# Kernel tuning notes

Hardware: AMD Instinct MI355X
Metric: run time of the kernel (lower is better)

## Reference

```python
import jax, jax.numpy as jnp
import numpy as np

B, NX, W, DX, DY, D, H, P = 8, 512, 16, 1536, 1024, 768, 12, 8


def setup_inputs() -> dict:
    key = jax.random.key(0)
    ks = jax.random.split(key, 12)
    r = lambda k, s: jax.random.normal(k, s, dtype=jnp.float32) * 0.02
    return {
        "x": jax.random.normal(ks[0], (B, NX, DX), jnp.float32),
        "y": jax.random.normal(ks[1], (B, NX * W, DY), jnp.float32),
        "Wx": r(ks[2], (DX, D)), "bx": jnp.zeros((D,), jnp.float32),
        "Wy": r(ks[3], (DY, D)), "by": jnp.zeros((D,), jnp.float32),
        "prompt": r(ks[4], (1, P, D)),
        "Wq": r(ks[5], (D, D)), "bq": jnp.zeros((D,), jnp.float32),
        "Wk": r(ks[6], (D, D)), "bk": jnp.zeros((D,), jnp.float32),
        "Wv": r(ks[7], (D, D)), "bv": jnp.zeros((D,), jnp.float32),
        "Wo": r(ks[8], (D, D)), "bo": jnp.zeros((D,), jnp.float32),
        "ln_g": jnp.ones((D,), jnp.float32), "ln_b": jnp.zeros((D,), jnp.float32),
    }


def _l2n(f, eps=1e-6):
    return f / (jnp.linalg.norm(f, axis=-1, keepdims=True) + eps)


def reference(x, y, Wx, bx, Wy, by, prompt, Wq, bq, Wk, bk, Wv, bv, Wo, bo, ln_g, ln_b):
    dh = D // H
    scale = 1.0 / jnp.sqrt(jnp.float32(dh))
    xp = _l2n(x @ Wx + bx)            # [B,NX,D]
    yp = _l2n(y @ Wy + by)            # [B,NX*W,D]
    # In the original, only normalized_output[:,0:1] is kept per window, and
    # per-query attention is independent, so only query index 0 contributes.
    q = ((xp[:, 0] @ Wq) + bq).reshape(B, H, dh) * scale   # [B,H,dh]
    yw = yp.reshape(B, NX, W, D)                            # 16-token windows
    k = ((yw @ Wk) + bk).reshape(B, NX, W, H, dh)
    v = ((yw @ Wv) + bv).reshape(B, NX, W, H, dh)
    s = jnp.einsum('bhd,bnwhd->bhnw', q, k)                # [B,H,NX,W]
    a = jax.nn.softmax(s, axis=-1)
    ctx = jnp.einsum('bhnw,bnwhd->bnhd', a, v).reshape(B, NX, D)
    o = ctx @ Wo + bo                                      # attn out_proj
    mu = jnp.mean(o, axis=-1, keepdims=True)
    var = jnp.var(o, axis=-1, keepdims=True)
    normed = (o - mu) / jnp.sqrt(var + 1e-6) * ln_g + ln_b  # [B,NX,D]
    blocks = jnp.concatenate(
        [normed[:, :, None, :],
         jnp.broadcast_to(prompt[:, None], (B, NX, P, D))], axis=2)  # [B,NX,1+P,D]
    return blocks.reshape(B, NX * (1 + P), D)
```

## Files before the change

kernel.cpp:

```cpp
#include <hip/hip_runtime.h>
#include <stdint.h>

#define BQ 8
#define NXQ 512
#define WQ 16
#define DXQ 1536
#define DYQ 1024
#define DQ 768
#define HQ 12
#define PQ 8
#define MY 65536
#define BN_ROWS 4096

typedef __attribute__((ext_vector_type(8))) short short8;
typedef __attribute__((ext_vector_type(4))) float f32x4;
typedef unsigned short ushort_t;
typedef unsigned int uint_t;

__device__ __forceinline__ ushort_t f2bf(float f) {
  uint_t u = __float_as_uint(f);
  u += 0x7FFFu + ((u >> 16) & 1u);
  return (ushort_t)(u >> 16);
}
__device__ __forceinline__ float bf2f(ushort_t h) {
  return __uint_as_float(((uint_t)h) << 16);
}
__device__ __forceinline__ void gload_lds16(const void* g, void* l) {
  __builtin_amdgcn_global_load_lds(
      (__attribute__((address_space(1))) unsigned int*)(g),
      (__attribute__((address_space(3))) unsigned int*)(l), 16, 0, 0);
}

__global__ void k_conv(const float* __restrict__ y, const float* __restrict__ Wy,
                       const float* __restrict__ Wv, const float* __restrict__ Wo,
                       ushort_t* __restrict__ ybf, ushort_t* __restrict__ WyT,
                       ushort_t* __restrict__ WvT, ushort_t* __restrict__ WoT,
                       float* __restrict__ rowsq, float* __restrict__ oS12,
                       float* __restrict__ xw) {
  const int gstride = gridDim.x * blockDim.x;
  const int g0 = blockIdx.x * blockDim.x + threadIdx.x;
  const int NY8 = MY * DYQ / 8;
  for (int i = g0; i < NY8; i += gstride) {
    const float4* s = (const float4*)(y + (size_t)i * 8);
    float4 f0 = s[0], f1 = s[1];
    short8 hv;
    hv[0] = (short)f2bf(f0.x); hv[1] = (short)f2bf(f0.y);
    hv[2] = (short)f2bf(f0.z); hv[3] = (short)f2bf(f0.w);
    hv[4] = (short)f2bf(f1.x); hv[5] = (short)f2bf(f1.y);
    hv[6] = (short)f2bf(f1.z); hv[7] = (short)f2bf(f1.w);
    *(short8*)(ybf + (size_t)i * 8) = hv;
  }
  for (int i = g0; i < MY; i += gstride) rowsq[i] = 0.f;
  for (int i = g0; i < 2 * BN_ROWS; i += gstride) oS12[i] = 0.f;
  for (int i = g0; i < BQ * DQ; i += gstride) xw[i] = 0.f;
  const int N1 = DQ * DYQ;
  const int N2 = DQ * DQ;
  const int total = N1 + 2 * N2;
  for (int i = g0; i < total; i += gstride) {
    if (i < N1) {
      int n = i / DYQ, k = i - n * DYQ;
      WyT[i] = f2bf(Wy[k * DQ + n]);
    } else if (i < N1 + N2) {
      int j = i - N1;
      int n = j / DQ, k = j - n * DQ;
      WvT[j] = f2bf(Wv[k * DQ + n]);
    } else {
      int j = i - N1 - N2;
      int n = j / DQ, k = j - n * DQ;
      WoT[j] = f2bf(Wo[k * DQ + n]);
    }
  }
}

__global__ __launch_bounds__(128) void k_q1(const float* __restrict__ x,
                                            const float* __restrict__ Wx,
                                            const float* __restrict__ bx,
                                            float* __restrict__ xw) {
  const int b = blockIdx.x, c = blockIdx.y * 128 + threadIdx.x;
  const int kc = blockIdx.z;
  const float* xr = x + (size_t)b * NXQ * DXQ + kc * 192;
  const float* wp = Wx + (size_t)kc * 192 * DQ + c;
  float acc = (kc == 0) ? bx[c] : 0.f;
  for (int k = 0; k < 192; ++k) acc += xr[k] * wp[(size_t)k * DQ];
  atomicAdd(&xw[b * DQ + c], acc);
}

__global__ __launch_bounds__(128) void k_q2(const float* __restrict__ xw,
                                            const float* __restrict__ Wq,
                                            const float* __restrict__ bq,
                                            float* __restrict__ qv) {
  const int b = blockIdx.x, c = blockIdx.y * 128 + threadIdx.x;
  const float* xr = xw + b * DQ;
  float acc = 0.f, ss = 0.f;
  for (int k = 0; k < DQ; ++k) {
    float v = xr[k];
    acc += v * Wq[(size_t)k * DQ + c];
    ss += v * v;
  }
  const float inv = 1.0f / (sqrtf(ss) + 1e-6f);
  qv[b * DQ + c] = (acc * inv + bq[c]) * 0.125f;
}

__global__ void k_q3(const float* __restrict__ Wk, const float* __restrict__ bk,
                     const float* __restrict__ qv, float* __restrict__ qk,
                     float* __restrict__ cQ) {
  const int bh = blockIdx.x;
  const int b = bh / HQ, h = bh - b * HQ;
  const int tid = threadIdx.x;
  const float* q = qv + b * DQ + h * 64;
#pragma unroll
  for (int j = 0; j < 3; ++j) {
    int dd = tid + j * 256;
    float acc = 0.f;
    for (int j2 = 0; j2 < 64; ++j2) acc += Wk[(size_t)dd * DQ + h * 64 + j2] * q[j2];
    qk[(size_t)bh * DQ + dd] = acc;
  }
  if (tid == 0) {
    float acc = 0.f;
    for (int j2 = 0; j2 < 64; ++j2) acc += q[j2] * bk[h * 64 + j2];
    cQ[bh] = acc;
  }
}

__global__ __launch_bounds__(512, 1) void k_gemm_yp(const ushort_t* __restrict__ ybf,
                                                    const ushort_t* __restrict__ WyT,
                                                    const float* __restrict__ by,
                                                    ushort_t* __restrict__ z,
                                                    float* __restrict__ rowsqg) {
  __shared__ __align__(16) char smem[131072 + 1024];
  float* rowsq_l = (float*)(smem + 131072);
  const int tid = threadIdx.x, lane = tid & 63, wv = tid >> 6;
  const int wvM = wv >> 2, wvN = wv & 3;
  const int g = blockIdx.x;
  const int m = (g / 24) * 8 + (g & 7);
  const int n = (g >> 3) % 3;
  const int mBase = m * 256, nBase = n * 256;
  if (tid < 256) rowsq_l[tid] = 0.f;

  const int sr = lane >> 2;
  const int sc = (lane & 3) ^ (sr & 3);
  const ushort_t* aQ[2]; const ushort_t* bQ[2];
  int qDst[2];
#pragma unroll
  for (int j = 0; j < 2; ++j) {
    int r = wv * 32 + j * 16 + sr;
    aQ[j] = ybf + (size_t)(mBase + r) * DYQ + sc * 8;
    bQ[j] = WyT + (size_t)(nBase + r) * DYQ + sc * 8;
    qDst[j] = (wv * 32 + j * 16) * 64;
  }
  const int q = lane >> 4;
  int aFr[8], bFr[4];
#pragma unroll
  for (int mf = 0; mf < 8; ++mf) {
    int r = wvM * 128 + mf * 16 + (lane & 15);
    aFr[mf] = r * 64 + ((q ^ (r & 3)) << 4);
  }
#pragma unroll
  for (int nf = 0; nf < 4; ++nf) {
    int r = wvN * 64 + nf * 16 + (lane & 15);
    bFr[nf] = 32768 + r * 64 + ((q ^ (r & 3)) << 4);
  }

#define YP_STAGE(bufb, tt, ks)                                                 \
  {                                                                            \
    char* db = smem + (bufb) * 65536 + (ks) * 16384;                           \
    _Pragma("unroll") for (int j = 0; j < 2; ++j)                              \
        gload_lds16(aQ[j] + (tt) * 64 + (ks) * 32, db + qDst[j]);              \
    _Pragma("unroll") for (int j = 0; j < 2; ++j)                              \
        gload_lds16(bQ[j] + (tt) * 64 + (ks) * 32, db + 32768 + qDst[j]);      \
  }

  f32x4 acc[8][4] = {};
  YP_STAGE(0, 0, 0);
  YP_STAGE(0, 0, 1);
  for (int t = 0; t < 16; ++t) {
    const int c = t & 1;
    const char* cb = smem + c * 65536;
#pragma unroll
    for (int ks = 0; ks < 2; ++ks) {
      if (t == 15 && ks == 1) {
        asm volatile("s_waitcnt vmcnt(0)" ::: "memory");
      } else {
        asm volatile("s_waitcnt vmcnt(4)" ::: "memory");
      }
      __builtin_amdgcn_s_barrier();
      __builtin_amdgcn_sched_barrier(0);
      short8 af[8], bf[4];
#pragma unroll
      for (int mf = 0; mf < 8; ++mf)
        af[mf] = *(const short8*)(cb + ks * 16384 + aFr[mf]);
#pragma unroll
      for (int nf = 0; nf < 4; ++nf)
        bf[nf] = *(const short8*)(cb + ks * 16384 + bFr[nf]);
      if (t < 15) YP_STAGE(c ^ 1, t + 1, ks);
      asm volatile("s_waitcnt lgkmcnt(0)" ::: "memory");
      __builtin_amdgcn_sched_barrier(0);
      __builtin_amdgcn_s_setprio(1);
#pragma unroll
      for (int nf = 0; nf < 4; ++nf)
#pragma unroll
        for (int mf = 0; mf < 8; ++mf)
          acc[mf][nf] = __builtin_amdgcn_mfma_f32_16x16x32_bf16(af[mf], bf[nf],
                                                                acc[mf][nf], 0, 0, 0);
      __builtin_amdgcn_s_setprio(0);
      __builtin_amdgcn_sched_barrier(0);
    }
  }
  __syncthreads();

  float byv[4];
#pragma unroll
  for (int nf = 0; nf < 4; ++nf) byv[nf] = by[nBase + wvN * 64 + nf * 16 + (lane & 15)];
#pragma unroll
  for (int mf = 0; mf < 8; ++mf) {
#pragma unroll
    for (int rr = 0; rr < 4; ++rr) {
      int row_l = wvM * 128 + mf * 16 + (lane >> 4) * 4 + rr;
      float ss = 0.f;
#pragma unroll
      for (int nf = 0; nf < 4; ++nf) {
        float zv = acc[mf][nf][rr] + byv[nf];
        ss += zv * zv;
        int col_l = wvN * 64 + nf * 16 + (lane & 15);
        *(ushort_t*)(smem + row_l * 512 + col_l * 2) = f2bf(zv);
      }
#pragma unroll
      for (int o = 1; o < 16; o <<= 1) ss += __shfl_xor(ss, o, 64);
      if ((lane & 15) == 0) atomicAdd(&rowsq_l[row_l], ss);
    }
  }
  __syncthreads();
  if (tid < 256) atomicAdd(&rowsqg[mBase + tid], rowsq_l[tid]);
#pragma unroll
  for (int it = 0; it < 16; ++it) {
    int row = it * 16 + (tid >> 5);
    int ch = tid & 31;
    uint4 v = *(const uint4*)(smem + row * 512 + ch * 16);
    *(uint4*)(z + (size_t)(mBase + row) * DQ + nBase + ch * 8) = v;
  }
}

__global__ __launch_bounds__(256) void k_attn(const ushort_t* __restrict__ z,
                                              const float* __restrict__ rowsqg,
                                              const float* __restrict__ qk,
                                              const float* __restrict__ cQ,
                                              ushort_t* __restrict__ p) {
  __shared__ __align__(16) char smem[16 * 1552 + 192 * 4 * 2 + 64];
  float* s_l = (float*)(smem + 16 * 1552);
  float* a_l = s_l + 192;
  float* inv_l = a_l + 192;
  const int bn = blockIdx.x, b = bn >> 9;
  const int tid = threadIdx.x;
  if (tid < 16) inv_l[tid] = 1.0f / (sqrtf(rowsqg[bn * 16 + tid]) + 1e-6f);
  for (int j = tid; j < 16 * 96; j += 256) {
    int w = j / 96, ch = j - w * 96;
    *(short8*)(smem + w * 1552 + ch * 16) =
        *(const short8*)(z + ((size_t)bn * 16 + w) * DQ + ch * 8);
  }
  __syncthreads();
  if (tid < 192) {
    int h = tid >> 4, w = tid & 15;
    const float4* qkp = (const float4*)(qk + (size_t)(b * HQ + h) * DQ);
    float acc = 0.f;
    const char* yrow = smem + w * 1552;
    for (int dc = 0; dc < 192; ++dc) {
      float4 q4 = qkp[dc];
      uint2 hh = *(const uint2*)(yrow + dc * 8);
      acc += q4.x * bf2f((ushort_t)(hh.x & 0xffff));
      acc += q4.y * bf2f((ushort_t)(hh.x >> 16));
      acc += q4.z * bf2f((ushort_t)(hh.y & 0xffff));
      acc += q4.w * bf2f((ushort_t)(hh.y >> 16));
    }
    s_l[tid] = acc * inv_l[w] + cQ[b * HQ + h];
  }
  __syncthreads();
  if (tid < 12) {
    float mx = -1e30f;
#pragma unroll
    for (int w = 0; w < 16; ++w) mx = fmaxf(mx, s_l[tid * 16 + w]);
    float sm = 0.f, ev[16];
#pragma unroll
    for (int w = 0; w < 16; ++w) {
      ev[w] = __expf(s_l[tid * 16 + w] - mx);
      sm += ev[w];
    }
    float rden = 1.0f / sm;
#pragma unroll
    for (int w = 0; w < 16; ++w) a_l[tid * 16 + w] = ev[w] * rden * inv_l[w];
  }
  __syncthreads();
  float zr[16][3];
#pragma unroll
  for (int w = 0; w < 16; ++w)
#pragma unroll
    for (int i = 0; i < 3; ++i)
      zr[w][i] = bf2f(*(const ushort_t*)(smem + w * 1552 + (tid + i * 256) * 2));
  for (int h = 0; h < HQ; ++h) {
    float acc0 = 0.f, acc1 = 0.f, acc2 = 0.f;
#pragma unroll
    for (int w = 0; w < 16; ++w) {
      float aw = a_l[h * 16 + w];
      acc0 += aw * zr[w][0];
      acc1 += aw * zr[w][1];
      acc2 += aw * zr[w][2];
    }
    size_t base = ((size_t)bn * HQ + h) * DQ + tid;
    p[base] = f2bf(acc0);
    p[base + 256] = f2bf(acc1);
    p[base + 512] = f2bf(acc2);
  }
}

#define PV_TSZ 24576
__global__ __launch_bounds__(256) void k_gemm_pv(const ushort_t* __restrict__ p,
                                                 const ushort_t* __restrict__ WvT,
                                                 const float* __restrict__ bv,
                                                 ushort_t* __restrict__ ctx) {
  __shared__ __align__(16) char smem[3 * PV_TSZ];
  const int tid = threadIdx.x, lane = tid & 63, wv = tid >> 6;
  const int wvM = wv >> 1, wvN = wv & 1;
  const int mBase = blockIdx.x * 128, h = blockIdx.y;
  const int l8 = lane >> 3;
  const int c8 = (lane & 7) ^ (l8 & 7);
  const ushort_t* aSrc[4]; const ushort_t* bSrc[2];
  int aDst[4], bDst[2];
#pragma unroll
  for (int j = 0; j < 4; ++j) {
    int r = wv * 32 + j * 8 + l8;
    aSrc[j] = p + ((size_t)(mBase + r) * HQ + h) * DQ + c8 * 8;
    aDst[j] = (wv * 32 + j * 8) * 128;
  }
#pragma unroll
  for (int j = 0; j < 2; ++j) {
    int r = wv * 16 + j * 8 + l8;
    bSrc[j] = WvT + (size_t)(h * 64 + r) * DQ + c8 * 8;
    bDst[j] = 16384 + (wv * 16 + j * 8) * 128;
  }
  const int q = lane >> 4;
  int aRowB[4], aSw[4], bRowB[2], bSw[2];
#pragma unroll
  for (int mf = 0; mf < 4; ++mf) {
    int r = wvM * 64 + mf * 16 + (lane & 15);
    aRowB[mf] = r * 128; aSw[mf] = r & 7;
  }
#pragma unroll
  for (int nf = 0; nf < 2; ++nf) {
    int r = wvN * 32 + nf * 16 + (lane & 15);
    bRowB[nf] = 16384 + r * 128; bSw[nf] = r & 7;
  }
#define PV_STAGE(dbuf, t)                                                      \
  {                                                                            \
    char* db = smem + (dbuf) * PV_TSZ;                                         \
    _Pragma("unroll") for (int j = 0; j < 4; ++j)                              \
        gload_lds16(aSrc[j] + (t) * 64, db + aDst[j]);                         \
    _Pragma("unroll") for (int j = 0; j < 2; ++j)                              \
        gload_lds16(bSrc[j] + (t) * 64, db + bDst[j]);                         \
  }
  f32x4 acc[4][2] = {};
  PV_STAGE(0, 0);
  PV_STAGE(1, 1);
  int bR = 0, bS = 2;
  for (int t = 0; t < 12; ++t) {
    if (t < 11) {
      asm volatile("s_waitcnt vmcnt(6)" ::: "memory");
    } else {
      asm volatile("s_waitcnt vmcnt(0)" ::: "memory");
    }
    __builtin_amdgcn_s_barrier();
    __builtin_amdgcn_sched_barrier(0);
    if (t + 2 < 12) PV_STAGE(bS, t + 2);
    const char* cur = smem + bR * PV_TSZ;
#pragma unroll
    for (int ks = 0; ks < 2; ++ks) {
      short8 af[4], bf[2];
#pragma unroll
      for (int mf = 0; mf < 4; ++mf)
        af[mf] = *(const short8*)(cur + aRowB[mf] + (((ks * 4 + q) ^ aSw[mf]) << 4));
#pragma unroll
      for (int nf = 0; nf < 2; ++nf)
        bf[nf] = *(const short8*)(cur + bRowB[nf] + (((ks * 4 + q) ^ bSw[nf]) << 4));
#pragma unroll
      for (int nf = 0; nf < 2; ++nf)
#pragma unroll
        for (int mf = 0; mf < 4; ++mf)
          acc[mf][nf] = __builtin_amdgcn_mfma_f32_16x16x32_bf16(af[mf], bf[nf],
                                                                acc[mf][nf], 0, 0, 0);
    }
    bR = (bR == 2) ? 0 : bR + 1;
    bS = (bS == 2) ? 0 : bS + 1;
  }
#pragma unroll
  for (int nf = 0; nf < 2; ++nf) {
    int col = h * 64 + wvN * 32 + nf * 16 + (lane & 15);
    float bvv = bv[col];
#pragma unroll
    for (int mf = 0; mf < 4; ++mf)
#pragma unroll
      for (int rr = 0; rr < 4; ++rr) {
        int row = mBase + wvM * 64 + mf * 16 + (lane >> 4) * 4 + rr;
        ctx[(size_t)row * DQ + col] = f2bf(acc[mf][nf][rr] + bvv);
      }
  }
}

__global__ __launch_bounds__(256) void k_gemm_o(const ushort_t* __restrict__ ctx,
                                                const ushort_t* __restrict__ WoT,
                                                const float* __restrict__ bo,
                                                float* __restrict__ o,
                                                float* __restrict__ oS12) {
  __shared__ __align__(16) char smem[3 * PV_TSZ];
  const int tid = threadIdx.x, lane = tid & 63, wv = tid >> 6;
  const int wvM = wv >> 1, wvN = wv & 1;
  const int mBase = blockIdx.x * 128, nBase = blockIdx.y * 64;
  const int l8 = lane >> 3;
  const int c8 = (lane & 7) ^ (l8 & 7);
  const ushort_t* aSrc[4]; const ushort_t* bSrc[2];
  int aDst[4], bDst[2];
#pragma unroll
  for (int j = 0; j < 4; ++j) {
    int r = wv * 32 + j * 8 + l8;
    aSrc[j] = ctx + (size_t)(mBase + r) * DQ + c8 * 8;
    aDst[j] = (wv * 32 + j * 8) * 128;
  }
#pragma unroll
  for (int j = 0; j < 2; ++j) {
    int r = wv * 16 + j * 8 + l8;
    bSrc[j] = WoT + (size_t)(nBase + r) * DQ + c8 * 8;
    bDst[j] = 16384 + (wv * 16 + j * 8) * 128;
  }
  const int q = lane >> 4;
  int aRowB[4], aSw[4], bRowB[2], bSw[2];
#pragma unroll
  for (int mf = 0; mf < 4; ++mf) {
    int r = wvM * 64 + mf * 16 + (lane & 15);
    aRowB[mf] = r * 128; aSw[mf] = r & 7;
  }
#pragma unroll
  for (int nf = 0; nf < 2; ++nf) {
    int r = wvN * 32 + nf * 16 + (lane & 15);
    bRowB[nf] = 16384 + r * 128; bSw[nf] = r & 7;
  }
  f32x4 acc[4][2] = {};
#define O_STAGE(dbuf, t)                                                       \
  {                                                                            \
    char* db = smem + (dbuf) * PV_TSZ;                                         \
    _Pragma("unroll") for (int j = 0; j < 4; ++j)                              \
        gload_lds16(aSrc[j] + (t) * 64, db + aDst[j]);                         \
    _Pragma("unroll") for (int j = 0; j < 2; ++j)                              \
        gload_lds16(bSrc[j] + (t) * 64, db + bDst[j]);                         \
  }
  O_STAGE(0, 0);
  O_STAGE(1, 1);
  int bR = 0, bS = 2;
  for (int t = 0; t < 12; ++t) {
    if (t < 11) {
      asm volatile("s_waitcnt vmcnt(6)" ::: "memory");
    } else {
      asm volatile("s_waitcnt vmcnt(0)" ::: "memory");
    }
    __builtin_amdgcn_s_barrier();
    __builtin_amdgcn_sched_barrier(0);
    if (t + 2 < 12) O_STAGE(bS, t + 2);
    const char* cur = smem + bR * PV_TSZ;
#pragma unroll
    for (int ks = 0; ks < 2; ++ks) {
      short8 af[4], bf[2];
#pragma unroll
      for (int mf = 0; mf < 4; ++mf)
        af[mf] = *(const short8*)(cur + aRowB[mf] + (((ks * 4 + q) ^ aSw[mf]) << 4));
#pragma unroll
      for (int nf = 0; nf < 2; ++nf)
        bf[nf] = *(const short8*)(cur + bRowB[nf] + (((ks * 4 + q) ^ bSw[nf]) << 4));
#pragma unroll
      for (int nf = 0; nf < 2; ++nf)
#pragma unroll
        for (int mf = 0; mf < 4; ++mf)
          acc[mf][nf] = __builtin_amdgcn_mfma_f32_16x16x32_bf16(af[mf], bf[nf],
                                                                acc[mf][nf], 0, 0, 0);
    }
    bR = (bR == 2) ? 0 : bR + 1;
    bS = (bS == 2) ? 0 : bS + 1;
  }
  float bo0 = bo[nBase + wvN * 32 + (lane & 15)];
  float bo1 = bo[nBase + wvN * 32 + 16 + (lane & 15)];
#pragma unroll
  for (int mf = 0; mf < 4; ++mf)
#pragma unroll
    for (int rr = 0; rr < 4; ++rr) {
      int row = mBase + wvM * 64 + mf * 16 + (lane >> 4) * 4 + rr;
      float z0 = acc[mf][0][rr] + bo0;
      float z1 = acc[mf][1][rr] + bo1;
      o[(size_t)row * DQ + nBase + wvN * 32 + (lane & 15)] = z0;
      o[(size_t)row * DQ + nBase + wvN * 32 + 16 + (lane & 15)] = z1;
      float s1 = z0 + z1, s2 = z0 * z0 + z1 * z1;
#pragma unroll
      for (int ofs = 1; ofs < 16; ofs <<= 1) {
        s1 += __shfl_xor(s1, ofs, 64);
        s2 += __shfl_xor(s2, ofs, 64);
      }
      if ((lane & 15) == 0) {
        atomicAdd(&oS12[row], s1);
        atomicAdd(&oS12[BN_ROWS + row], s2);
      }
    }
}

__global__ __launch_bounds__(256) void k_out(const float* __restrict__ o,
                                             const float* __restrict__ oS12,
                                             const float* __restrict__ ln_g,
                                             const float* __restrict__ ln_b,
                                             const float* __restrict__ prompt,
                                             float* __restrict__ out) {
  const int row = blockIdx.x;
  const int tid = threadIdx.x;
  float mu = oS12[row] * (1.0f / DQ);
  float va = oS12[BN_ROWS + row] * (1.0f / DQ) - mu * mu;
  float rstd = rsqrtf(va + 1e-6f);
  int b = row >> 9, n = row & 511;
  size_t obase = ((size_t)b * (NXQ * (PQ + 1)) + (size_t)n * (PQ + 1)) * DQ;
#pragma unroll
  for (int j = 0; j < 3; ++j) {
    int col = tid + j * 256;
    out[obase + col] = (o[(size_t)row * DQ + col] - mu) * rstd * ln_g[col] + ln_b[col];
  }
#pragma unroll
  for (int pi = 0; pi < PQ; ++pi)
#pragma unroll
    for (int j = 0; j < 3; ++j) {
      int col = tid + j * 256;
      out[obase + (size_t)(1 + pi) * DQ + col] = prompt[pi * DQ + col];
    }
}

extern "C" void kernel_launch(void* const* d_in, const int* in_sizes, int n_in,
                              void* d_out, int out_size, void* d_ws, size_t ws_size,
                              hipStream_t stream) {
  (void)in_sizes; (void)n_in; (void)out_size; (void)ws_size;
  const float* x    = (const float*)d_in[0];
  const float* y    = (const float*)d_in[1];
  const float* Wx   = (const float*)d_in[2];
  const float* bx   = (const float*)d_in[3];
  const float* Wy   = (const float*)d_in[4];
  const float* by   = (const float*)d_in[5];
  const float* prom = (const float*)d_in[6];
  const float* Wq   = (const float*)d_in[7];
  const float* bq   = (const float*)d_in[8];
  const float* Wk   = (const float*)d_in[9];
  const float* bk   = (const float*)d_in[10];
  const float* Wv   = (const float*)d_in[11];
  const float* bv   = (const float*)d_in[12];
  const float* Wo   = (const float*)d_in[13];
  const float* bo   = (const float*)d_in[14];
  const float* lng  = (const float*)d_in[15];
  const float* lnb  = (const float*)d_in[16];
  float* out = (float*)d_out;
  char* ws = (char*)d_ws;

  size_t oWyT = 0;
  size_t oWvT = oWyT + (size_t)DQ * DYQ * 2;
  size_t oWoT = oWvT + (size_t)DQ * DQ * 2;
  size_t oXw  = oWoT + (size_t)DQ * DQ * 2;
  size_t oQ   = oXw + (size_t)BQ * DQ * 4 + 256;
  size_t oQK  = oQ + (size_t)BQ * DQ * 4;
  size_t oC   = oQK + (size_t)BQ * HQ * DQ * 4;
  size_t oRq  = oC + 1024;
  size_t oS   = oRq + (size_t)MY * 4;
  size_t oYbf = oS + (size_t)2 * BN_ROWS * 4;
  size_t oZ   = oYbf + (size_t)MY * DYQ * 2;
  size_t oP   = oYbf;
  size_t oCtx = oYbf + (size_t)BN_ROWS * HQ * DQ * 2;
  size_t oO   = oZ;

  ushort_t* WyT = (ushort_t*)(ws + oWyT);
  ushort_t* WvT = (ushort_t*)(ws + oWvT);
  ushort_t* WoT = (ushort_t*)(ws + oWoT);
  float* xw  = (float*)(ws + oXw);
  float* qv  = (float*)(ws + oQ);
  float* qk  = (float*)(ws + oQK);
  float* cQ  = (float*)(ws + oC);
  float* rowsq = (float*)(ws + oRq);
  float* oS12  = (float*)(ws + oS);
  ushort_t* ybf  = (ushort_t*)(ws + oYbf);
  ushort_t* zbuf = (ushort_t*)(ws + oZ);
  ushort_t* p    = (ushort_t*)(ws + oP);
  ushort_t* ctx  = (ushort_t*)(ws + oCtx);
  float* obuf    = (float*)(ws + oO);

  k_conv<<<dim3(4096), dim3(256), 0, stream>>>(y, Wy, Wv, Wo, ybf, WyT, WvT, WoT,
                                               rowsq, oS12, xw);
  k_q1<<<dim3(BQ, 6, 8), dim3(128), 0, stream>>>(x, Wx, bx, xw);
  k_q2<<<dim3(BQ, 6), dim3(128), 0, stream>>>(xw, Wq, bq, qv);
  k_q3<<<dim3(BQ * HQ), dim3(256), 0, stream>>>(Wk, bk, qv, qk, cQ);
  k_gemm_yp<<<dim3(768), dim3(512), 0, stream>>>(ybf, WyT, by, zbuf, rowsq);
  k_attn<<<dim3(BN_ROWS), dim3(256), 0, stream>>>(zbuf, rowsq, qk, cQ, p);
  k_gemm_pv<<<dim3(BN_ROWS / 128, HQ), dim3(256), 0, stream>>>(p, WvT, bv, ctx);
  k_gemm_o<<<dim3(BN_ROWS / 128, DQ / 64), dim3(256), 0, stream>>>(ctx, WoT, bo, obuf, oS12);
  k_out<<<dim3(BN_ROWS), dim3(256), 0, stream>>>(obuf, oS12, lng, lnb, prom, out);
}
```

Measured before the change: 450.7 us.

## Deepen yp GEMM LDS pipeline to four-stage ring with three loads in flight

Replaces the two-buffer (double-buffered, two k-substeps each) LDS scheme in the y-projection GEMM with a four-slot ring of 32 KB half-steps. Loads are issued three stages ahead, and the wait-plus-barrier moves to after the MFMA block. The goal is to hide more global-load latency behind MFMA work. The prefetch buffer footprint stays the same, but the vmcnt bookkeeping is more complex and each step still needs a barrier.

```diff
diff --git a/kernel.cpp b/kernel.cpp
--- a/kernel.cpp
+++ b/kernel.cpp
@@ -158,41 +158,38 @@
 #pragma unroll
   for (int nf = 0; nf < 4; ++nf) {
     int r = wvN * 64 + nf * 16 + (lane & 15);
-    bFr[nf] = 32768 + r * 64 + ((q ^ (r & 3)) << 4);
-  }
-
-#define YP_STAGE(bufb, tt, ks)                                                 \
+    bFr[nf] = 16384 + r * 64 + ((q ^ (r & 3)) << 4);
+  }
+
+#define YP_STAGE(pp)                                                           \
   {                                                                            \
-    char* db = smem + (bufb) * 65536 + (ks) * 16384;                           \
+    char* db = smem + ((pp) & 3) * 32768;                                      \
+    const int koff = ((pp) >> 1) * 64 + ((pp) & 1) * 32;                       \
     _Pragma("unroll") for (int j = 0; j < 2; ++j)                              \
-        gload_lds16(aQ[j] + (tt) * 64 + (ks) * 32, db + qDst[j]);              \
+        gload_lds16(aQ[j] + koff, db + qDst[j]);                               \
     _Pragma("unroll") for (int j = 0; j < 2; ++j)                              \
-        gload_lds16(bQ[j] + (tt) * 64 + (ks) * 32, db + 32768 + qDst[j]);      \
+        gload_lds16(bQ[j] + koff, db + 16384 + qDst[j]);                       \
   }
 
   f32x4 acc[8][4] = {};
-  YP_STAGE(0, 0, 0);
-  YP_STAGE(0, 0, 1);
+  YP_STAGE(0);
+  YP_STAGE(1);
+  YP_STAGE(2);
+  asm volatile("s_waitcnt vmcnt(8)" ::: "memory");
+  __builtin_amdgcn_s_barrier();
+  __builtin_amdgcn_sched_barrier(0);
+
   for (int t = 0; t < 16; ++t) {
-    const int c = t & 1;
-    const char* cb = smem + c * 65536;
 #pragma unroll
     for (int ks = 0; ks < 2; ++ks) {
-      if (t == 15 && ks == 1) {
-        asm volatile("s_waitcnt vmcnt(0)" ::: "memory");
-      } else {
-        asm volatile("s_waitcnt vmcnt(4)" ::: "memory");
-      }
-      __builtin_amdgcn_s_barrier();
-      __builtin_amdgcn_sched_barrier(0);
+      const int p = 2 * t + ks;
+      const char* cb = smem + (p & 3) * 32768;
       short8 af[8], bf[4];
 #pragma unroll
-      for (int mf = 0; mf < 8; ++mf)
-        af[mf] = *(const short8*)(cb + ks * 16384 + aFr[mf]);
-#pragma unroll
-      for (int nf = 0; nf < 4; ++nf)
-        bf[nf] = *(const short8*)(cb + ks * 16384 + bFr[nf]);
-      if (t < 15) YP_STAGE(c ^ 1, t + 1, ks);
+      for (int mf = 0; mf < 8; ++mf) af[mf] = *(const short8*)(cb + aFr[mf]);
+#pragma unroll
+      for (int nf = 0; nf < 4; ++nf) bf[nf] = *(const short8*)(cb + bFr[nf]);
+      if (p <= 28) YP_STAGE(p + 3);
       asm volatile("s_waitcnt lgkmcnt(0)" ::: "memory");
       __builtin_amdgcn_sched_barrier(0);
       __builtin_amdgcn_s_setprio(1);
@@ -203,6 +200,15 @@
           acc[mf][nf] = __builtin_amdgcn_mfma_f32_16x16x32_bf16(af[mf], bf[nf],
                                                                 acc[mf][nf], 0, 0, 0);
       __builtin_amdgcn_s_setprio(0);
+      __builtin_amdgcn_sched_barrier(0);
+      if (p <= 28) {
+        asm volatile("s_waitcnt vmcnt(8)" ::: "memory");
+      } else if (p == 29) {
+        asm volatile("s_waitcnt vmcnt(4)" ::: "memory");
+      } else {
+        asm volatile("s_waitcnt vmcnt(0)" ::: "memory");
+      }
+      __builtin_amdgcn_s_barrier();
       __builtin_amdgcn_sched_barrier(0);
     }
   }
```

Result: no change. 446.9 us (-0.8%).
